# Performance work log

Hardware: AMD Instinct MI355X
Metric: run time of the kernel (lower is better)

The kernel has to match this reference:

```python
import jax, jax.numpy as jnp
import numpy as np

N_NODES = 100000
N_EDGES = 1600000
D_IN, D_HID, D_OUT = 512, 256, 40
DROPOUT_P = 0.5


def setup_inputs() -> dict:
    key = jax.random.key(0)
    ks = jax.random.split(key, 8)
    x = jax.random.normal(ks[0], (N_NODES, D_IN), dtype=jnp.float32)
    edge_src = jax.random.randint(ks[1], (N_EDGES,), 0, N_NODES, dtype=jnp.int32)
    edge_dst = jax.random.randint(ks[2], (N_EDGES,), 0, N_NODES, dtype=jnp.int32)
    edge_weight = jax.random.uniform(ks[3], (N_EDGES,), dtype=jnp.float32)
    W1 = jax.random.normal(ks[4], (D_IN, D_HID), dtype=jnp.float32) * (1.0 / np.sqrt(D_IN))
    b1 = jax.random.normal(ks[5], (D_HID,), dtype=jnp.float32) * 0.01
    W2 = jax.random.normal(ks[6], (D_HID, D_OUT), dtype=jnp.float32) * (1.0 / np.sqrt(D_HID))
    b2 = jax.random.normal(ks[7], (D_OUT,), dtype=jnp.float32) * 0.01
    return {"x": x, "edge_src": edge_src, "edge_dst": edge_dst, "edge_weight": edge_weight,
            "W1": W1, "b1": b1, "W2": W2, "b2": b2}


def _graph_conv(x, src, dst, ew, W, b):
    # support = x @ W  (dense GEMM), then spmm: out[d] = sum_e ew[e] * support[src[e]]
    support = x @ W                                  # [N, F_out]
    msgs = support[src] * ew[:, None]                # [E, F_out] gather + scale
    return jax.ops.segment_sum(msgs, dst, num_segments=N_NODES) + b


def reference(x, edge_src, edge_dst, edge_weight, W1, b1, W2, b2):
    h = jax.nn.relu(_graph_conv(x, edge_src, edge_dst, edge_weight, W1, b1))
    # dropout (train mode, fixed key for determinism), inverted scaling
    keep = jax.random.bernoulli(jax.random.key(42), 1.0 - DROPOUT_P, h.shape)
    h = jnp.where(keep, h / (1.0 - DROPOUT_P), 0.0)
    logits = _graph_conv(h, edge_src, edge_dst, edge_weight, W2, b2)
    return jax.nn.log_softmax(logits, axis=1)
```

## Files before the change

### kernel.cpp

```cpp
#include <hip/hip_runtime.h>
#include <math.h>

#define N_NODES 100000
#define N_EDGES 1600000
#define D_IN 512
#define D_HID 256
#define D_OUT 40
#define S2_LD 48
#define SCAN_BLOCKS ((N_NODES + 255) / 256)

typedef short short8 __attribute__((ext_vector_type(8)));
typedef short short4v __attribute__((ext_vector_type(4)));
typedef float f32x4 __attribute__((ext_vector_type(4)));

static __device__ __forceinline__ short f2bf(float f) {
  unsigned u = __float_as_uint(f);
  u = (u + 0x7fffu + ((u >> 16) & 1u)) >> 16;
  return (short)u;
}
static __device__ __forceinline__ float bf2f(unsigned short h) {
  return __uint_as_float(((unsigned)h) << 16);
}

static __device__ __forceinline__ void threefry_0_42(unsigned x0, unsigned x1,
                                                     unsigned& o0, unsigned& o1) {
  const unsigned ks0 = 0u;
  const unsigned ks1 = 42u;
  const unsigned ks2 = 0u ^ 42u ^ 0x1BD11BDAu;
  x0 += ks0; x1 += ks1;
#define TF_R(r) { x0 += x1; x1 = (x1 << (r)) | (x1 >> (32 - (r))); x1 ^= x0; }
  TF_R(13) TF_R(15) TF_R(26) TF_R(6)
  x0 += ks1; x1 += ks2 + 1u;
  TF_R(17) TF_R(29) TF_R(16) TF_R(24)
  x0 += ks2; x1 += ks0 + 2u;
  TF_R(13) TF_R(15) TF_R(26) TF_R(6)
  x0 += ks0; x1 += ks1 + 3u;
  TF_R(17) TF_R(29) TF_R(16) TF_R(24)
  x0 += ks1; x1 += ks2 + 4u;
  TF_R(13) TF_R(15) TF_R(26) TF_R(6)
  x0 += ks2; x1 += ks0 + 5u;
#undef TF_R
  o0 = x0; o1 = x1;
}

__global__ __launch_bounds__(256) void hist_kernel(const int* __restrict__ edst,
                                                   int* __restrict__ counts) {
  const int e = blockIdx.x * 256 + threadIdx.x;
  if (e < N_EDGES) atomicAdd(&counts[edst[e]], 1);
}

__global__ __launch_bounds__(256) void block_sum_kernel(const int* __restrict__ counts,
                                                        int* __restrict__ bsums) {
  __shared__ int red[256];
  const int t = threadIdx.x;
  const int i = blockIdx.x * 256 + t;
  red[t] = (i < N_NODES) ? counts[i] : 0;
  __syncthreads();
#pragma unroll
  for (int off = 128; off > 0; off >>= 1) {
    if (t < off) red[t] += red[t + off];
    __syncthreads();
  }
  if (t == 0) bsums[blockIdx.x] = red[0];
}

__global__ __launch_bounds__(512) void bsum_scan_kernel(const int* __restrict__ bsums,
                                                        int* __restrict__ boffs) {
  __shared__ int tmp[512];
  const int t = threadIdx.x;
  const int v = (t < SCAN_BLOCKS) ? bsums[t] : 0;
  tmp[t] = v;
  __syncthreads();
  for (int off = 1; off < 512; off <<= 1) {
    const int add = (t >= off) ? tmp[t - off] : 0;
    __syncthreads();
    tmp[t] += add;
    __syncthreads();
  }
  if (t < SCAN_BLOCKS) boffs[t] = tmp[t] - v;
}

__global__ __launch_bounds__(256) void scan_apply_kernel(const int* __restrict__ counts,
                                                         const int* __restrict__ boffs,
                                                         int* __restrict__ rowptr,
                                                         int* __restrict__ cursor) {
  __shared__ int tmp[256];
  const int t = threadIdx.x;
  const int i = blockIdx.x * 256 + t;
  const int v = (i < N_NODES) ? counts[i] : 0;
  tmp[t] = v;
  __syncthreads();
  for (int off = 1; off < 256; off <<= 1) {
    const int add = (t >= off) ? tmp[t - off] : 0;
    __syncthreads();
    tmp[t] += add;
    __syncthreads();
  }
  const int excl = boffs[blockIdx.x] + tmp[t] - v;
  if (i < N_NODES) {
    rowptr[i] = excl;
    cursor[i] = excl;
    if (i == N_NODES - 1) rowptr[N_NODES] = excl + v;
  }
}

__global__ __launch_bounds__(256) void scatter_kernel(const int* __restrict__ esrc,
                                                      const int* __restrict__ edst,
                                                      const float* __restrict__ ew,
                                                      int* __restrict__ cursor,
                                                      int2* __restrict__ pairs) {
  const int e = blockIdx.x * 256 + threadIdx.x;
  if (e >= N_EDGES) return;
  const int d = edst[e];
  const int pos = atomicAdd(&cursor[d], 1);
  int2 p;
  p.x = esrc[e];
  p.y = __float_as_int(ew[e]);
  pairs[pos] = p;
}

__global__ __launch_bounds__(256) void w1t_kernel(const float* __restrict__ W1,
                                                  short* __restrict__ W1t) {
  const int i = blockIdx.x * 256 + threadIdx.x;
  if (i >= D_IN * D_HID) return;
  const int n = i >> 9;
  const int k = i & 511;
  W1t[i] = f2bf(W1[(size_t)k * D_HID + n]);
}

__global__ __launch_bounds__(256) void w2t_kernel(const float* __restrict__ W2,
                                                  short* __restrict__ W2t) {
  const int i = blockIdx.x * 256 + threadIdx.x;
  if (i >= 48 * D_HID) return;
  const int n = i >> 8;
  const int k = i & 255;
  W2t[i] = (n < D_OUT) ? f2bf(W2[(size_t)k * D_OUT + n]) : (short)0;
}

__global__ __launch_bounds__(512) void gemm1_mfma_kernel(const float* __restrict__ x,
                                                         const short* __restrict__ W1t,
                                                         short* __restrict__ out) {
  __shared__ __attribute__((aligned(16))) short As[128][40];
  __shared__ __attribute__((aligned(16))) short Bs[256][40];

  const int tid  = threadIdx.x;
  const int lane = tid & 63;
  const int wid  = tid >> 6;
  const int wm   = wid >> 2;
  const int wn   = wid & 3;
  const int lr   = lane & 15;
  const int lg   = lane >> 4;
  const int row0 = blockIdx.x * 128;

  f32x4 acc[4][4] = {};

  for (int kt = 0; kt < D_IN; kt += 32) {
    {
      const int m  = tid >> 2;
      const int kc = tid & 3;
      short8 v;
      const int grow = row0 + m;
      if (grow < N_NODES) {
        const float* src = x + (size_t)grow * D_IN + kt + kc * 8;
        const float4 f0 = *(const float4*)(src);
        const float4 f1 = *(const float4*)(src + 4);
        v[0] = f2bf(f0.x); v[1] = f2bf(f0.y); v[2] = f2bf(f0.z); v[3] = f2bf(f0.w);
        v[4] = f2bf(f1.x); v[5] = f2bf(f1.y); v[6] = f2bf(f1.z); v[7] = f2bf(f1.w);
      } else {
        v = (short8)0;
      }
      *(short8*)&As[m][kc * 8] = v;
    }
    {
#pragma unroll
      for (int c = 0; c < 2; ++c) {
        const int t2 = (tid << 1) | c;
        const int n  = t2 >> 2;
        const int kc = t2 & 3;
        const short8 v = *(const short8*)(W1t + (size_t)n * D_IN + kt + kc * 8);
        *(short8*)&Bs[n][kc * 8] = v;
      }
    }
    __syncthreads();

    short8 a[4], b[4];
#pragma unroll
    for (int mi = 0; mi < 4; ++mi)
      a[mi] = *(const short8*)&As[wm * 64 + mi * 16 + lr][lg * 8];
#pragma unroll
    for (int nj = 0; nj < 4; ++nj)
      b[nj] = *(const short8*)&Bs[wn * 64 + nj * 16 + lr][lg * 8];

#pragma unroll
    for (int mi = 0; mi < 4; ++mi)
#pragma unroll
      for (int nj = 0; nj < 4; ++nj)
        acc[mi][nj] = __builtin_amdgcn_mfma_f32_16x16x32_bf16(a[mi], b[nj], acc[mi][nj], 0, 0, 0);

    __syncthreads();
  }

#pragma unroll
  for (int mi = 0; mi < 4; ++mi) {
#pragma unroll
    for (int nj = 0; nj < 4; ++nj) {
      const int gcol = wn * 64 + nj * 16 + lr;
#pragma unroll
      for (int r = 0; r < 4; ++r) {
        const int grow = row0 + wm * 64 + mi * 16 + lg * 4 + r;
        if (grow < N_NODES) out[(size_t)grow * D_HID + gcol] = f2bf(acc[mi][nj][r]);
      }
    }
  }
}

__global__ __launch_bounds__(256) void spmm1_csr_kernel(const short* __restrict__ sup,
                                                        const int* __restrict__ rowptr,
                                                        const int2* __restrict__ pairs,
                                                        const float* __restrict__ b1,
                                                        short* __restrict__ h) {
  const int node = blockIdx.x * 4 + (threadIdx.x >> 6);
  const int lane = threadIdx.x & 63;
  const int half = lane >> 5;
  const int hl   = lane & 31;
  if (node >= N_NODES) return;
  const int beg = rowptr[node];
  const int end = rowptr[node + 1];

  float acc[8] = {};

  int e = beg + half;
  for (; e + 6 < end; e += 8) {
    const int2 p0 = pairs[e];
    const int2 p1 = pairs[e + 2];
    const int2 p2 = pairs[e + 4];
    const int2 p3 = pairs[e + 6];
    const short8 v0 = *(const short8*)(sup + (size_t)p0.x * D_HID + hl * 8);
    const short8 v1 = *(const short8*)(sup + (size_t)p1.x * D_HID + hl * 8);
    const short8 v2 = *(const short8*)(sup + (size_t)p2.x * D_HID + hl * 8);
    const short8 v3 = *(const short8*)(sup + (size_t)p3.x * D_HID + hl * 8);
    const float w0 = __int_as_float(p0.y);
    const float w1 = __int_as_float(p1.y);
    const float w2 = __int_as_float(p2.y);
    const float w3 = __int_as_float(p3.y);
#pragma unroll
    for (int j = 0; j < 8; ++j) acc[j] += w0 * bf2f((unsigned short)v0[j]);
#pragma unroll
    for (int j = 0; j < 8; ++j) acc[j] += w1 * bf2f((unsigned short)v1[j]);
#pragma unroll
    for (int j = 0; j < 8; ++j) acc[j] += w2 * bf2f((unsigned short)v2[j]);
#pragma unroll
    for (int j = 0; j < 8; ++j) acc[j] += w3 * bf2f((unsigned short)v3[j]);
  }
  for (; e < end; e += 2) {
    const int2 p0 = pairs[e];
    const float w0 = __int_as_float(p0.y);
    const short8 v0 = *(const short8*)(sup + (size_t)p0.x * D_HID + hl * 8);
#pragma unroll
    for (int j = 0; j < 8; ++j) acc[j] += w0 * bf2f((unsigned short)v0[j]);
  }

#pragma unroll
  for (int j = 0; j < 8; ++j) acc[j] += __shfl_xor(acc[j], 32, 64);

  const int col = hl * 8 + half * 4;
  short4v r;
#pragma unroll
  for (int j = 0; j < 4; ++j) {
    float v = acc[half * 4 + j] + b1[col + j];
    v = v > 0.0f ? v : 0.0f;
    unsigned o0, o1;
    threefry_0_42(0u, (unsigned)node * D_HID + col + j, o0, o1);
    const unsigned word = o0 ^ o1;
    r[j] = (word >> 31) ? (short)0 : f2bf(v * 2.0f);
  }
  *(short4v*)(h + (size_t)node * D_HID + col) = r;
}

__global__ __launch_bounds__(256) void gemm2_mfma_kernel(const short* __restrict__ h,
                                                         const short* __restrict__ W2t,
                                                         float* __restrict__ out) {
  __shared__ __attribute__((aligned(16))) short As[128][40];
  __shared__ __attribute__((aligned(16))) short Bs[48][40];

  const int tid  = threadIdx.x;
  const int lane = tid & 63;
  const int wm   = tid >> 6;
  const int lr   = lane & 15;
  const int lg   = lane >> 4;
  const int row0 = blockIdx.x * 128;

  f32x4 acc[2][3] = {};

  for (int kt = 0; kt < D_HID; kt += 32) {
    {
#pragma unroll
      for (int c = 0; c < 2; ++c) {
        const int t2 = (tid << 1) | c;
        const int m  = t2 >> 2;
        const int kc = t2 & 3;
        const int grow = row0 + m;
        short8 v = (short8)0;
        if (grow < N_NODES)
          v = *(const short8*)(h + (size_t)grow * D_HID + kt + kc * 8);
        *(short8*)&As[m][kc * 8] = v;
      }
    }
    if (tid < 192) {
      const int n  = tid >> 2;
      const int kc = tid & 3;
      const short8 v = *(const short8*)(W2t + (size_t)n * D_HID + kt + kc * 8);
      *(short8*)&Bs[n][kc * 8] = v;
    }
    __syncthreads();

    short8 a[2], b[3];
#pragma unroll
    for (int mi = 0; mi < 2; ++mi)
      a[mi] = *(const short8*)&As[wm * 32 + mi * 16 + lr][lg * 8];
#pragma unroll
    for (int nj = 0; nj < 3; ++nj)
      b[nj] = *(const short8*)&Bs[nj * 16 + lr][lg * 8];

#pragma unroll
    for (int mi = 0; mi < 2; ++mi)
#pragma unroll
      for (int nj = 0; nj < 3; ++nj)
        acc[mi][nj] = __builtin_amdgcn_mfma_f32_16x16x32_bf16(a[mi], b[nj], acc[mi][nj], 0, 0, 0);

    __syncthreads();
  }

#pragma unroll
  for (int mi = 0; mi < 2; ++mi) {
#pragma unroll
    for (int nj = 0; nj < 3; ++nj) {
      const int gcol = nj * 16 + lr;
      if (gcol < D_OUT) {
#pragma unroll
        for (int r = 0; r < 4; ++r) {
          const int grow = row0 + wm * 32 + mi * 16 + lg * 4 + r;
          if (grow < N_NODES) out[(size_t)grow * S2_LD + gcol] = acc[mi][nj][r];
        }
      }
    }
  }
}

__global__ __launch_bounds__(256) void spmm2_csr_kernel(const float* __restrict__ sup2,
                                                        const int* __restrict__ rowptr,
                                                        const int2* __restrict__ pairs,
                                                        const float* __restrict__ b2,
                                                        float* __restrict__ out) {
  const int node = blockIdx.x * 4 + (threadIdx.x >> 6);
  const int lane = threadIdx.x & 63;
  if (node >= N_NODES) return;
  const int beg = rowptr[node];
  const int end = rowptr[node + 1];
  const bool act = lane < D_OUT;

  float a0 = 0.f, a1 = 0.f, a2 = 0.f, a3 = 0.f;
  int e = beg;
  for (; e + 4 <= end; e += 4) {
    const int2 p0 = pairs[e], p1 = pairs[e + 1], p2 = pairs[e + 2], p3 = pairs[e + 3];
    if (act) {
      const float v0 = sup2[(size_t)p0.x * S2_LD + lane];
      const float v1 = sup2[(size_t)p1.x * S2_LD + lane];
      const float v2 = sup2[(size_t)p2.x * S2_LD + lane];
      const float v3 = sup2[(size_t)p3.x * S2_LD + lane];
      a0 += __int_as_float(p0.y) * v0;
      a1 += __int_as_float(p1.y) * v1;
      a2 += __int_as_float(p2.y) * v2;
      a3 += __int_as_float(p3.y) * v3;
    }
  }
  for (; e < end; ++e) {
    const int2 p0 = pairs[e];
    if (act) a0 += __int_as_float(p0.y) * sup2[(size_t)p0.x * S2_LD + lane];
  }
  float acc = (a0 + a1) + (a2 + a3);

  float v = act ? acc + b2[lane] : -INFINITY;
  float m = v;
#pragma unroll
  for (int off = 32; off > 0; off >>= 1) m = fmaxf(m, __shfl_xor(m, off, 64));
  float ex = act ? expf(v - m) : 0.0f;
  float s = ex;
#pragma unroll
  for (int off = 32; off > 0; off >>= 1) s += __shfl_xor(s, off, 64);
  if (act) out[(size_t)node * D_OUT + lane] = v - m - logf(s);
}

extern "C" void kernel_launch(void* const* d_in, const int* in_sizes, int n_in,
                              void* d_out, int out_size, void* d_ws, size_t ws_size,
                              hipStream_t stream) {
  const float* x    = (const float*)d_in[0];
  const int*   esrc = (const int*)d_in[1];
  const int*   edst = (const int*)d_in[2];
  const float* ew   = (const float*)d_in[3];
  const float* W1   = (const float*)d_in[4];
  const float* b1   = (const float*)d_in[5];
  const float* W2   = (const float*)d_in[6];
  const float* b2   = (const float*)d_in[7];
  float* out = (float*)d_out;

  float* ws = (float*)d_ws;
  short* support1 = (short*)ws;
  short* hbuf     = (short*)(ws + 12800000);
  float* support2 = ws + 25600000;
  int2*  pairs    = (int2*)(ws + 30400000);
  int*   rowptr   = (int*)(ws + 33600000);
  int*   counts   = (int*)(ws + 33700008);
  int*   cursor   = (int*)(ws + 33800008);
  short* W1t      = (short*)(ws + 33900008);
  short* W2t      = (short*)(ws + 33965544);
  int*   bsums    = (int*)(ws + 33971688);
  int*   boffs    = bsums + 512;

  hipMemsetAsync(counts, 0, N_NODES * sizeof(int), stream);

  hist_kernel<<<(N_EDGES + 255) / 256, 256, 0, stream>>>(edst, counts);
  w1t_kernel<<<(D_IN * D_HID + 255) / 256, 256, 0, stream>>>(W1, W1t);
  w2t_kernel<<<(48 * D_HID + 255) / 256, 256, 0, stream>>>(W2, W2t);
  block_sum_kernel<<<SCAN_BLOCKS, 256, 0, stream>>>(counts, bsums);
  bsum_scan_kernel<<<1, 512, 0, stream>>>(bsums, boffs);
  scan_apply_kernel<<<SCAN_BLOCKS, 256, 0, stream>>>(counts, boffs, rowptr, cursor);
  scatter_kernel<<<(N_EDGES + 255) / 256, 256, 0, stream>>>(esrc, edst, ew, cursor, pairs);

  gemm1_mfma_kernel<<<(N_NODES + 127) / 128, 512, 0, stream>>>(x, W1t, support1);
  spmm1_csr_kernel<<<(N_NODES + 3) / 4, 256, 0, stream>>>(support1, rowptr, pairs, b1, hbuf);

  gemm2_mfma_kernel<<<(N_NODES + 127) / 128, 256, 0, stream>>>(hbuf, W2t, support2);
  spmm2_csr_kernel<<<(N_NODES + 3) / 4, 256, 0, stream>>>(support2, rowptr, pairs, b2, out);
}
```

Measured before the change: 473.2 us.

## Store layer-2 support in bf16 and process two nodes per wave in spmm2

Layer-2 support is now written as bf16 instead of fp32, which halves the bytes gathered per edge in the second SpMM. spmm2 now maps two nodes to each 64-lane wave, with each lane handling two output columns through 32-bit loads, and it uses __expf. The two weight-transpose kernels are merged into one launch. The cost is reduced precision of support2 before aggregation and log-softmax.

```diff
diff --git a/kernel.cpp b/kernel.cpp
--- a/kernel.cpp
+++ b/kernel.cpp
@@ -119,22 +119,23 @@
   pairs[pos] = p;
 }
 
-__global__ __launch_bounds__(256) void w1t_kernel(const float* __restrict__ W1,
-                                                  short* __restrict__ W1t) {
+__global__ __launch_bounds__(256) void wprep_kernel(const float* __restrict__ W1,
+                                                    const float* __restrict__ W2,
+                                                    short* __restrict__ W1t,
+                                                    short* __restrict__ W2t) {
   const int i = blockIdx.x * 256 + threadIdx.x;
-  if (i >= D_IN * D_HID) return;
-  const int n = i >> 9;
-  const int k = i & 511;
-  W1t[i] = f2bf(W1[(size_t)k * D_HID + n]);
-}
-
-__global__ __launch_bounds__(256) void w2t_kernel(const float* __restrict__ W2,
-                                                  short* __restrict__ W2t) {
-  const int i = blockIdx.x * 256 + threadIdx.x;
-  if (i >= 48 * D_HID) return;
-  const int n = i >> 8;
-  const int k = i & 255;
-  W2t[i] = (n < D_OUT) ? f2bf(W2[(size_t)k * D_OUT + n]) : (short)0;
+  if (i < D_IN * D_HID) {
+    const int n = i >> 9;
+    const int k = i & 511;
+    W1t[i] = f2bf(W1[(size_t)k * D_HID + n]);
+  } else {
+    const int j = i - D_IN * D_HID;
+    if (j < 48 * D_HID) {
+      const int n = j >> 8;
+      const int k = j & 255;
+      W2t[j] = (n < D_OUT) ? f2bf(W2[(size_t)k * D_OUT + n]) : (short)0;
+    }
+  }
 }
 
 __global__ __launch_bounds__(512) void gemm1_mfma_kernel(const float* __restrict__ x,
@@ -279,7 +280,7 @@
 
 __global__ __launch_bounds__(256) void gemm2_mfma_kernel(const short* __restrict__ h,
                                                          const short* __restrict__ W2t,
-                                                         float* __restrict__ out) {
+                                                         short* __restrict__ out) {
   __shared__ __attribute__((aligned(16))) short As[128][40];
   __shared__ __attribute__((aligned(16))) short Bs[48][40];
 
@@ -340,55 +341,73 @@
 #pragma unroll
         for (int r = 0; r < 4; ++r) {
           const int grow = row0 + wm * 32 + mi * 16 + lg * 4 + r;
-          if (grow < N_NODES) out[(size_t)grow * S2_LD + gcol] = acc[mi][nj][r];
+          if (grow < N_NODES) out[(size_t)grow * S2_LD + gcol] = f2bf(acc[mi][nj][r]);
         }
       }
     }
   }
 }
 
-__global__ __launch_bounds__(256) void spmm2_csr_kernel(const float* __restrict__ sup2,
+__global__ __launch_bounds__(256) void spmm2_csr_kernel(const short* __restrict__ sup2,
                                                         const int* __restrict__ rowptr,
                                                         const int2* __restrict__ pairs,
                                                         const float* __restrict__ b2,
                                                         float* __restrict__ out) {
-  const int node = blockIdx.x * 4 + (threadIdx.x >> 6);
   const int lane = threadIdx.x & 63;
+  const int half = lane >> 5;
+  const int hl   = lane & 31;
+  const int node = blockIdx.x * 8 + ((threadIdx.x >> 6) << 1) + half;
   if (node >= N_NODES) return;
   const int beg = rowptr[node];
   const int end = rowptr[node + 1];
-  const bool act = lane < D_OUT;
-
-  float a0 = 0.f, a1 = 0.f, a2 = 0.f, a3 = 0.f;
+  const bool act = hl < 20;
+
+  float a0 = 0.f, a1 = 0.f, b0 = 0.f, b1 = 0.f;
+  float c0 = 0.f, c1 = 0.f, d0 = 0.f, d1 = 0.f;
   int e = beg;
   for (; e + 4 <= end; e += 4) {
     const int2 p0 = pairs[e], p1 = pairs[e + 1], p2 = pairs[e + 2], p3 = pairs[e + 3];
     if (act) {
-      const float v0 = sup2[(size_t)p0.x * S2_LD + lane];
-      const float v1 = sup2[(size_t)p1.x * S2_LD + lane];
-      const float v2 = sup2[(size_t)p2.x * S2_LD + lane];
-      const float v3 = sup2[(size_t)p3.x * S2_LD + lane];
-      a0 += __int_as_float(p0.y) * v0;
-      a1 += __int_as_float(p1.y) * v1;
-      a2 += __int_as_float(p2.y) * v2;
-      a3 += __int_as_float(p3.y) * v3;
+      const unsigned u0 = *(const unsigned*)(sup2 + (size_t)p0.x * S2_LD + hl * 2);
+      const unsigned u1 = *(const unsigned*)(sup2 + (size_t)p1.x * S2_LD + hl * 2);
+      const unsigned u2 = *(const unsigned*)(sup2 + (size_t)p2.x * S2_LD + hl * 2);
+      const unsigned u3 = *(const unsigned*)(sup2 + (size_t)p3.x * S2_LD + hl * 2);
+      const float w0 = __int_as_float(p0.y);
+      const float w1 = __int_as_float(p1.y);
+      const float w2 = __int_as_float(p2.y);
+      const float w3 = __int_as_float(p3.y);
+      a0 += w0 * bf2f((unsigned short)(u0 & 0xffff)); a1 += w0 * bf2f((unsigned short)(u0 >> 16));
+      b0 += w1 * bf2f((unsigned short)(u1 & 0xffff)); b1 += w1 * bf2f((unsigned short)(u1 >> 16));
+      c0 += w2 * bf2f((unsigned short)(u2 & 0xffff)); c1 += w2 * bf2f((unsigned short)(u2 >> 16));
+      d0 += w3 * bf2f((unsigned short)(u3 & 0xffff)); d1 += w3 * bf2f((unsigned short)(u3 >> 16));
     }
   }
   for (; e < end; ++e) {
     const int2 p0 = pairs[e];
-    if (act) a0 += __int_as_float(p0.y) * sup2[(size_t)p0.x * S2_LD + lane];
-  }
-  float acc = (a0 + a1) + (a2 + a3);
-
-  float v = act ? acc + b2[lane] : -INFINITY;
-  float m = v;
-#pragma unroll
-  for (int off = 32; off > 0; off >>= 1) m = fmaxf(m, __shfl_xor(m, off, 64));
-  float ex = act ? expf(v - m) : 0.0f;
-  float s = ex;
-#pragma unroll
-  for (int off = 32; off > 0; off >>= 1) s += __shfl_xor(s, off, 64);
-  if (act) out[(size_t)node * D_OUT + lane] = v - m - logf(s);
+    if (act) {
+      const unsigned u0 = *(const unsigned*)(sup2 + (size_t)p0.x * S2_LD + hl * 2);
+      const float w0 = __int_as_float(p0.y);
+      a0 += w0 * bf2f((unsigned short)(u0 & 0xffff)); a1 += w0 * bf2f((unsigned short)(u0 >> 16));
+    }
+  }
+  const float f0 = (a0 + b0) + (c0 + d0);
+  const float f1 = (a1 + b1) + (c1 + d1);
+
+  const float v0 = act ? f0 + b2[hl * 2]     : -INFINITY;
+  const float v1 = act ? f1 + b2[hl * 2 + 1] : -INFINITY;
+  float m = fmaxf(v0, v1);
+#pragma unroll
+  for (int off = 16; off > 0; off >>= 1) m = fmaxf(m, __shfl_xor(m, off, 32));
+  float s = act ? __expf(v0 - m) + __expf(v1 - m) : 0.0f;
+#pragma unroll
+  for (int off = 16; off > 0; off >>= 1) s += __shfl_xor(s, off, 32);
+  if (act) {
+    const float ls = logf(s);
+    float2 r;
+    r.x = v0 - m - ls;
+    r.y = v1 - m - ls;
+    *(float2*)&out[(size_t)node * D_OUT + hl * 2] = r;
+  }
 }
 
 extern "C" void kernel_launch(void* const* d_in, const int* in_sizes, int n_in,
@@ -407,7 +426,7 @@
   float* ws = (float*)d_ws;
   short* support1 = (short*)ws;
   short* hbuf     = (short*)(ws + 12800000);
-  float* support2 = ws + 25600000;
+  short* support2 = (short*)(ws + 25600000);
   int2*  pairs    = (int2*)(ws + 30400000);
   int*   rowptr   = (int*)(ws + 33600000);
   int*   counts   = (int*)(ws + 33700008);
@@ -420,8 +439,7 @@
   hipMemsetAsync(counts, 0, N_NODES * sizeof(int), stream);
 
   hist_kernel<<<(N_EDGES + 255) / 256, 256, 0, stream>>>(edst, counts);
-  w1t_kernel<<<(D_IN * D_HID + 255) / 256, 256, 0, stream>>>(W1, W1t);
-  w2t_kernel<<<(48 * D_HID + 255) / 256, 256, 0, stream>>>(W2, W2t);
+  wprep_kernel<<<(D_IN * D_HID + 48 * D_HID + 255) / 256, 256, 0, stream>>>(W1, W2, W1t, W2t);
   block_sum_kernel<<<SCAN_BLOCKS, 256, 0, stream>>>(counts, bsums);
   bsum_scan_kernel<<<1, 512, 0, stream>>>(bsums, boffs);
   scan_apply_kernel<<<SCAN_BLOCKS, 256, 0, stream>>>(counts, boffs, rowptr, cursor);
@@ -431,5 +449,5 @@
   spmm1_csr_kernel<<<(N_NODES + 3) / 4, 256, 0, stream>>>(support1, rowptr, pairs, b1, hbuf);
 
   gemm2_mfma_kernel<<<(N_NODES + 127) / 128, 256, 0, stream>>>(hbuf, W2t, support2);
-  spmm2_csr_kernel<<<(N_NODES + 3) / 4, 256, 0, stream>>>(support2, rowptr, pairs, b2, out);
-}
+  spmm2_csr_kernel<<<(N_NODES + 7) / 8, 256, 0, stream>>>(support2, rowptr, pairs, b2, out);
+}
```

After: 451.6 us. -4.6%, faster.
